# Kernel optimization log

Hardware: AMD Instinct MI355X
Metric: run time of the kernel (lower is better)

Reference implementation:

```python
import jax, jax.numpy as jnp
import numpy as np

EPS = 1e-5


def setup_inputs() -> dict:
    key = jax.random.key(0)
    k1, k2, k3, k4 = jax.random.split(key, 4)
    B, C, H, W = 32, 256, 64, 64
    x_real = jax.random.normal(k1, (B, C, H, W), dtype=jnp.float32)
    x_imag = jax.random.normal(k2, (B, C, H, W), dtype=jnp.float32)
    # per-channel 2x2 affine weight and 2-vector bias (module init is
    # 0.7071*I and zeros; we perturb so gradients are non-trivial)
    weight = (0.70710678 * jnp.eye(2, dtype=jnp.float32)[:, :, None]
              + 0.05 * jax.random.normal(k3, (2, 2, C), dtype=jnp.float32))
    bias = 0.05 * jax.random.normal(k4, (2, C), dtype=jnp.float32)
    return {"x_real": x_real, "x_imag": x_imag, "weight": weight, "bias": bias}


def reference(x_real, x_imag, weight, bias):
    # Complex BatchNorm (training-mode batch statistics).
    # x_*: [B, C, H, W]; stats reduced over (B, H, W) per channel C.
    axes = (0, 2, 3)
    mu_r = jnp.mean(x_real, axes)  # [C]
    mu_i = jnp.mean(x_imag, axes)  # [C]
    xr = x_real - mu_r[None, :, None, None]
    xi = x_imag - mu_i[None, :, None, None]

    # 2x2 covariance per channel, eps on the diagonal
    Vrr = jnp.mean(xr * xr, axes) + EPS  # [C]
    Vii = jnp.mean(xi * xi, axes) + EPS  # [C]
    Vri = jnp.mean(xr * xi, axes)        # [C]

    # Analytic inverse square root of the 2x2 SPD matrix [[Vrr,Vri],[Vri,Vii]]
    s = jnp.sqrt(Vrr * Vii - Vri * Vri)       # sqrt(det)
    t = jnp.sqrt(Vrr + Vii + 2.0 * s)         # sqrt(trace + 2 sqrt(det))
    inv_st = 1.0 / (s * t)
    Rrr = (Vii + s) * inv_st
    Rii = (Vrr + s) * inv_st
    Rri = -Vri * inv_st

    # Whitening (per-channel 2x2 matmul on (real, imag))
    cb = lambda v: v[None, :, None, None]
    xhat_r = cb(Rrr) * xr + cb(Rri) * xi
    xhat_i = cb(Rri) * xr + cb(Rii) * xi

    # Affine: out = W @ xhat + b, W: [2,2,C], b: [2,C]
    out_r = cb(weight[0, 0]) * xhat_r + cb(weight[0, 1]) * xhat_i + cb(bias[0])
    out_i = cb(weight[1, 0]) * xhat_r + cb(weight[1, 1]) * xhat_i + cb(bias[1])
    return jnp.stack([out_r, out_i], axis=0)  # [2, B, C, H, W]
```

## Files before the change

kernel.cpp:

```cpp
#include <hip/hip_runtime.h>
#include <math.h>

#define C_CH   256
#define HW     4096
#define B_N    32
#define N_PER_CH (B_N * HW)
#define N_TOT  ((size_t)B_N * C_CH * HW)
#define EPS_BN 1e-5f

typedef float f32x4 __attribute__((ext_vector_type(4)));

__global__ __launch_bounds__(1024) void cbn_fused(
    const float* __restrict__ xr, const float* __restrict__ xi,
    const float* __restrict__ weight,
    const float* __restrict__ bias,
    float* __restrict__ out)
{
    const int c = blockIdx.x;
    const int t = threadIdx.x;
    const f32x4* r4 = reinterpret_cast<const f32x4*>(xr);
    const f32x4* i4 = reinterpret_cast<const f32x4*>(xi);

    float sr = 0.f, si = 0.f, srr = 0.f, sii = 0.f, sri = 0.f;
#pragma unroll 4
    for (int j = 0; j < B_N; ++j) {
        const size_t idx = ((size_t)(j * C_CH + c) << 10) + t;
        const f32x4 a = r4[idx];
        const f32x4 b = i4[idx];
        sr  += a.x + a.y + a.z + a.w;
        si  += b.x + b.y + b.z + b.w;
        srr += a.x * a.x + a.y * a.y + a.z * a.z + a.w * a.w;
        sii += b.x * b.x + b.y * b.y + b.z * b.z + b.w * b.w;
        sri += a.x * b.x + a.y * b.y + a.z * b.z + a.w * b.w;
    }

#pragma unroll
    for (int off = 32; off > 0; off >>= 1) {
        sr  += __shfl_down(sr,  off);
        si  += __shfl_down(si,  off);
        srr += __shfl_down(srr, off);
        sii += __shfl_down(sii, off);
        sri += __shfl_down(sri, off);
    }

    __shared__ float red[5][16];
    __shared__ float scoef[6];
    const int wave = t >> 6;
    if ((t & 63) == 0) {
        red[0][wave] = sr;  red[1][wave] = si;
        red[2][wave] = srr; red[3][wave] = sii; red[4][wave] = sri;
    }
    __syncthreads();

    if (t < 64) {
        float v0 = 0.f, v1 = 0.f, v2 = 0.f, v3 = 0.f, v4 = 0.f;
        if (t < 16) {
            v0 = red[0][t]; v1 = red[1][t]; v2 = red[2][t];
            v3 = red[3][t]; v4 = red[4][t];
        }
#pragma unroll
        for (int off = 8; off > 0; off >>= 1) {
            v0 += __shfl_down(v0, off);
            v1 += __shfl_down(v1, off);
            v2 += __shfl_down(v2, off);
            v3 += __shfl_down(v3, off);
            v4 += __shfl_down(v4, off);
        }
        if (t == 0) {
            const float invN = 1.0f / (float)N_PER_CH;
            const float mur = v0 * invN;
            const float mui = v1 * invN;
            const float Vrr = v2 * invN - mur * mur + EPS_BN;
            const float Vii = v3 * invN - mui * mui + EPS_BN;
            const float Vri = v4 * invN - mur * mui;

            const float s      = sqrtf(Vrr * Vii - Vri * Vri);
            const float tt     = sqrtf(Vrr + Vii + 2.0f * s);
            const float inv_st = 1.0f / (s * tt);
            const float Rrr = (Vii + s) * inv_st;
            const float Rii = (Vrr + s) * inv_st;
            const float Rri = -Vri * inv_st;

            const float w00 = weight[0 * C_CH + c];
            const float w01 = weight[1 * C_CH + c];
            const float w10 = weight[2 * C_CH + c];
            const float w11 = weight[3 * C_CH + c];
            const float b0  = bias[c];
            const float b1  = bias[C_CH + c];

            const float Ar = w00 * Rrr + w01 * Rri;
            const float Br = w00 * Rri + w01 * Rii;
            const float Ai = w10 * Rrr + w11 * Rri;
            const float Bi = w10 * Rri + w11 * Rii;

            scoef[0] = Ar;
            scoef[1] = Br;
            scoef[2] = b0 - Ar * mur - Br * mui;
            scoef[3] = Ai;
            scoef[4] = Bi;
            scoef[5] = b1 - Ai * mur - Bi * mui;
        }
    }
    __syncthreads();

    const float Ar = scoef[0], Br = scoef[1], Cr = scoef[2];
    const float Ai = scoef[3], Bi = scoef[4], Ci = scoef[5];

    f32x4* o4 = reinterpret_cast<f32x4*>(out);
    const size_t n4 = N_TOT / 4;

#pragma unroll 4
    for (int j = 0; j < B_N; ++j) {
        const size_t idx = ((size_t)(j * C_CH + c) << 10) + t;
        const f32x4 a = __builtin_nontemporal_load(&r4[idx]);
        const f32x4 b = __builtin_nontemporal_load(&i4[idx]);
        f32x4 u, v;
        u.x = Ar * a.x + Br * b.x + Cr;
        u.y = Ar * a.y + Br * b.y + Cr;
        u.z = Ar * a.z + Br * b.z + Cr;
        u.w = Ar * a.w + Br * b.w + Cr;
        v.x = Ai * a.x + Bi * b.x + Ci;
        v.y = Ai * a.y + Bi * b.y + Ci;
        v.z = Ai * a.z + Bi * b.z + Ci;
        v.w = Ai * a.w + Bi * b.w + Ci;
        __builtin_nontemporal_store(u, &o4[idx]);
        __builtin_nontemporal_store(v, &o4[n4 + idx]);
    }
}

extern "C" void kernel_launch(void* const* d_in, const int* in_sizes, int n_in,
                              void* d_out, int out_size, void* d_ws, size_t ws_size,
                              hipStream_t stream) {
    const float* xr     = (const float*)d_in[0];
    const float* xi     = (const float*)d_in[1];
    const float* weight = (const float*)d_in[2];
    const float* bias   = (const float*)d_in[3];
    float* out = (float*)d_out;

    cbn_fused<<<C_CH, 1024, 0, stream>>>(xr, xi, weight, bias, out);
}
```

Measured before the change: 121.1 us.

## Keep part of each channel's input in registers and LDS between stats and apply passes

The first 10 batch slices per thread are held in registers and the next 4 in shared memory across the statistics pass, so the apply pass re-reads only the remaining 18 slices from global memory. This cuts second-pass HBM/L2 reads by roughly 14/32. In exchange it uses about 80 VGPRs of f32x4 for the cached slices and 128KB of LDS per block. With only 256 blocks of 1024 threads, occupancy is likely limited already, but the register pressure could force spills.

```diff
diff --git a/kernel.cpp b/kernel.cpp
--- a/kernel.cpp
+++ b/kernel.cpp
@@ -8,9 +8,12 @@
 #define N_TOT  ((size_t)B_N * C_CH * HW)
 #define EPS_BN 1e-5f
 
+#define JR 10
+#define JL 4
+
 typedef float f32x4 __attribute__((ext_vector_type(4)));
 
-__global__ __launch_bounds__(1024) void cbn_fused(
+__global__ __launch_bounds__(1024, 4) void cbn_fused(
     const float* __restrict__ xr, const float* __restrict__ xi,
     const float* __restrict__ weight,
     const float* __restrict__ bias,
@@ -21,9 +24,40 @@
     const f32x4* r4 = reinterpret_cast<const f32x4*>(xr);
     const f32x4* i4 = reinterpret_cast<const f32x4*>(xi);
 
+    __shared__ f32x4 lr[JL][1024];
+    __shared__ f32x4 li[JL][1024];
+    __shared__ float red[5][16];
+    __shared__ float scoef[6];
+
     float sr = 0.f, si = 0.f, srr = 0.f, sii = 0.f, sri = 0.f;
-#pragma unroll 4
-    for (int j = 0; j < B_N; ++j) {
+    f32x4 ra[JR], ia[JR];
+
+#pragma unroll
+    for (int j = 0; j < JR; ++j) {
+        const size_t idx = ((size_t)(j * C_CH + c) << 10) + t;
+        const f32x4 a = __builtin_nontemporal_load(&r4[idx]);
+        const f32x4 b = __builtin_nontemporal_load(&i4[idx]);
+        ra[j] = a; ia[j] = b;
+        sr  += a.x + a.y + a.z + a.w;
+        si  += b.x + b.y + b.z + b.w;
+        srr += a.x * a.x + a.y * a.y + a.z * a.z + a.w * a.w;
+        sii += b.x * b.x + b.y * b.y + b.z * b.z + b.w * b.w;
+        sri += a.x * b.x + a.y * b.y + a.z * b.z + a.w * b.w;
+    }
+#pragma unroll
+    for (int j = 0; j < JL; ++j) {
+        const size_t idx = ((size_t)((JR + j) * C_CH + c) << 10) + t;
+        const f32x4 a = __builtin_nontemporal_load(&r4[idx]);
+        const f32x4 b = __builtin_nontemporal_load(&i4[idx]);
+        lr[j][t] = a; li[j][t] = b;
+        sr  += a.x + a.y + a.z + a.w;
+        si  += b.x + b.y + b.z + b.w;
+        srr += a.x * a.x + a.y * a.y + a.z * a.z + a.w * a.w;
+        sii += b.x * b.x + b.y * b.y + b.z * b.z + b.w * b.w;
+        sri += a.x * b.x + a.y * b.y + a.z * b.z + a.w * b.w;
+    }
+#pragma unroll 2
+    for (int j = JR + JL; j < B_N; ++j) {
         const size_t idx = ((size_t)(j * C_CH + c) << 10) + t;
         const f32x4 a = r4[idx];
         const f32x4 b = i4[idx];
@@ -42,9 +76,6 @@
         sii += __shfl_down(sii, off);
         sri += __shfl_down(sri, off);
     }
-
-    __shared__ float red[5][16];
-    __shared__ float scoef[6];
     const int wave = t >> 6;
     if ((t & 63) == 0) {
         red[0][wave] = sr;  red[1][wave] = si;
@@ -109,8 +140,42 @@
     f32x4* o4 = reinterpret_cast<f32x4*>(out);
     const size_t n4 = N_TOT / 4;
 
-#pragma unroll 4
-    for (int j = 0; j < B_N; ++j) {
+#pragma unroll
+    for (int j = 0; j < JR; ++j) {
+        const size_t idx = ((size_t)(j * C_CH + c) << 10) + t;
+        const f32x4 a = ra[j];
+        const f32x4 b = ia[j];
+        f32x4 u, v;
+        u.x = Ar * a.x + Br * b.x + Cr;
+        u.y = Ar * a.y + Br * b.y + Cr;
+        u.z = Ar * a.z + Br * b.z + Cr;
+        u.w = Ar * a.w + Br * b.w + Cr;
+        v.x = Ai * a.x + Bi * b.x + Ci;
+        v.y = Ai * a.y + Bi * b.y + Ci;
+        v.z = Ai * a.z + Bi * b.z + Ci;
+        v.w = Ai * a.w + Bi * b.w + Ci;
+        __builtin_nontemporal_store(u, &o4[idx]);
+        __builtin_nontemporal_store(v, &o4[n4 + idx]);
+    }
+#pragma unroll
+    for (int j = 0; j < JL; ++j) {
+        const size_t idx = ((size_t)((JR + j) * C_CH + c) << 10) + t;
+        const f32x4 a = lr[j][t];
+        const f32x4 b = li[j][t];
+        f32x4 u, v;
+        u.x = Ar * a.x + Br * b.x + Cr;
+        u.y = Ar * a.y + Br * b.y + Cr;
+        u.z = Ar * a.z + Br * b.z + Cr;
+        u.w = Ar * a.w + Br * b.w + Cr;
+        v.x = Ai * a.x + Bi * b.x + Ci;
+        v.y = Ai * a.y + Bi * b.y + Ci;
+        v.z = Ai * a.z + Bi * b.z + Ci;
+        v.w = Ai * a.w + Bi * b.w + Ci;
+        __builtin_nontemporal_store(u, &o4[idx]);
+        __builtin_nontemporal_store(v, &o4[n4 + idx]);
+    }
+#pragma unroll 2
+    for (int j = JR + JL; j < B_N; ++j) {
         const size_t idx = ((size_t)(j * C_CH + c) << 10) + t;
         const f32x4 a = __builtin_nontemporal_load(&r4[idx]);
         const f32x4 b = __builtin_nontemporal_load(&i4[idx]);
```

After: 132.1 us. +9.0%, slower.

## Split channels into groups and pipeline stats and apply across five launches

Applied to the files above, without the earlier changes.

Replaces the single fused kernel (one 1024-thread block per channel) with five launches of 256 blocks of 512 threads. Each launch applies the normalization to one group of 64 channels while computing statistics for the next group. Each channel's statistics are split across 4 blocks and combined through a workspace buffer. The aim is to use more blocks and to reuse data while it is still in L2/MALL: the stats pass touches a group, and the apply pass reads that same group one launch later. In exchange it adds four extra kernel launch boundaries and depends on the workspace.

```diff
diff --git a/kernel.cpp b/kernel.cpp
--- a/kernel.cpp
+++ b/kernel.cpp
@@ -8,65 +8,42 @@
 #define N_TOT  ((size_t)B_N * C_CH * HW)
 #define EPS_BN 1e-5f
 
+#define GCH    64
+#define QS     8
+#define NT     512
+
 typedef float f32x4 __attribute__((ext_vector_type(4)));
 
-__global__ __launch_bounds__(1024) void cbn_fused(
+__global__ __launch_bounds__(NT) void cbn_epoch(
     const float* __restrict__ xr, const float* __restrict__ xi,
     const float* __restrict__ weight,
     const float* __restrict__ bias,
-    float* __restrict__ out)
+    float* __restrict__ out,
+    float* __restrict__ part,
+    const int apply_g, const int stats_g)
 {
-    const int c = blockIdx.x;
-    const int t = threadIdx.x;
+    const int blk = blockIdx.x;
+    const int t   = threadIdx.x;
     const f32x4* r4 = reinterpret_cast<const f32x4*>(xr);
     const f32x4* i4 = reinterpret_cast<const f32x4*>(xi);
 
-    float sr = 0.f, si = 0.f, srr = 0.f, sii = 0.f, sri = 0.f;
-#pragma unroll 4
-    for (int j = 0; j < B_N; ++j) {
-        const size_t idx = ((size_t)(j * C_CH + c) << 10) + t;
-        const f32x4 a = r4[idx];
-        const f32x4 b = i4[idx];
-        sr  += a.x + a.y + a.z + a.w;
-        si  += b.x + b.y + b.z + b.w;
-        srr += a.x * a.x + a.y * a.y + a.z * a.z + a.w * a.w;
-        sii += b.x * b.x + b.y * b.y + b.z * b.z + b.w * b.w;
-        sri += a.x * b.x + a.y * b.y + a.z * b.z + a.w * b.w;
-    }
+    __shared__ float sp[20];
+    __shared__ float scoef[6];
+    __shared__ float red[5][8];
 
-#pragma unroll
-    for (int off = 32; off > 0; off >>= 1) {
-        sr  += __shfl_down(sr,  off);
-        si  += __shfl_down(si,  off);
-        srr += __shfl_down(srr, off);
-        sii += __shfl_down(sii, off);
-        sri += __shfl_down(sri, off);
-    }
+    if (apply_g >= 0) {
+        const int ch = apply_g * GCH + (blk >> 2);
+        const int q  = blk & 3;
 
-    __shared__ float red[5][16];
-    __shared__ float scoef[6];
-    const int wave = t >> 6;
-    if ((t & 63) == 0) {
-        red[0][wave] = sr;  red[1][wave] = si;
-        red[2][wave] = srr; red[3][wave] = sii; red[4][wave] = sri;
-    }
-    __syncthreads();
+        if (t < 20) sp[t] = part[ch * 20 + t];
+        __syncthreads();
+        if (t == 0) {
+            const float v0 = sp[0] + sp[5]  + sp[10] + sp[15];
+            const float v1 = sp[1] + sp[6]  + sp[11] + sp[16];
+            const float v2 = sp[2] + sp[7]  + sp[12] + sp[17];
+            const float v3 = sp[3] + sp[8]  + sp[13] + sp[18];
+            const float v4 = sp[4] + sp[9]  + sp[14] + sp[19];
 
-    if (t < 64) {
-        float v0 = 0.f, v1 = 0.f, v2 = 0.f, v3 = 0.f, v4 = 0.f;
-        if (t < 16) {
-            v0 = red[0][t]; v1 = red[1][t]; v2 = red[2][t];
-            v3 = red[3][t]; v4 = red[4][t];
-        }
-#pragma unroll
-        for (int off = 8; off > 0; off >>= 1) {
-            v0 += __shfl_down(v0, off);
-            v1 += __shfl_down(v1, off);
-            v2 += __shfl_down(v2, off);
-            v3 += __shfl_down(v3, off);
-            v4 += __shfl_down(v4, off);
-        }
-        if (t == 0) {
             const float invN = 1.0f / (float)N_PER_CH;
             const float mur = v0 * invN;
             const float mui = v1 * invN;
@@ -81,12 +58,12 @@
             const float Rii = (Vrr + s) * inv_st;
             const float Rri = -Vri * inv_st;
 
-            const float w00 = weight[0 * C_CH + c];
-            const float w01 = weight[1 * C_CH + c];
-            const float w10 = weight[2 * C_CH + c];
-            const float w11 = weight[3 * C_CH + c];
-            const float b0  = bias[c];
-            const float b1  = bias[C_CH + c];
+            const float w00 = weight[0 * C_CH + ch];
+            const float w01 = weight[1 * C_CH + ch];
+            const float w10 = weight[2 * C_CH + ch];
+            const float w11 = weight[3 * C_CH + ch];
+            const float b0  = bias[ch];
+            const float b1  = bias[C_CH + ch];
 
             const float Ar = w00 * Rrr + w01 * Rri;
             const float Br = w00 * Rri + w01 * Rii;
@@ -100,31 +77,81 @@
             scoef[4] = Bi;
             scoef[5] = b1 - Ai * mur - Bi * mui;
         }
+        __syncthreads();
+
+        const float Ar = scoef[0], Br = scoef[1], Cr = scoef[2];
+        const float Ai = scoef[3], Bi = scoef[4], Ci = scoef[5];
+
+        f32x4* o4 = reinterpret_cast<f32x4*>(out);
+        const size_t n4 = N_TOT / 4;
+
+#pragma unroll 2
+        for (int j = q * QS; j < q * QS + QS; ++j) {
+            const size_t base = ((size_t)(j * C_CH + ch) << 10);
+#pragma unroll
+            for (int k = 0; k < 2; ++k) {
+                const size_t idx = base + (size_t)k * NT + t;
+                const f32x4 a = __builtin_nontemporal_load(&r4[idx]);
+                const f32x4 b = __builtin_nontemporal_load(&i4[idx]);
+                f32x4 u, v;
+                u.x = Ar * a.x + Br * b.x + Cr;
+                u.y = Ar * a.y + Br * b.y + Cr;
+                u.z = Ar * a.z + Br * b.z + Cr;
+                u.w = Ar * a.w + Br * b.w + Cr;
+                v.x = Ai * a.x + Bi * b.x + Ci;
+                v.y = Ai * a.y + Bi * b.y + Ci;
+                v.z = Ai * a.z + Bi * b.z + Ci;
+                v.w = Ai * a.w + Bi * b.w + Ci;
+                __builtin_nontemporal_store(u, &o4[idx]);
+                __builtin_nontemporal_store(v, &o4[n4 + idx]);
+            }
+        }
     }
-    __syncthreads();
 
-    const float Ar = scoef[0], Br = scoef[1], Cr = scoef[2];
-    const float Ai = scoef[3], Bi = scoef[4], Ci = scoef[5];
+    if (stats_g >= 0) {
+        const int ch = stats_g * GCH + (blk >> 2);
+        const int q  = blk & 3;
 
-    f32x4* o4 = reinterpret_cast<f32x4*>(out);
-    const size_t n4 = N_TOT / 4;
+        float sr = 0.f, si = 0.f, srr = 0.f, sii = 0.f, sri = 0.f;
+#pragma unroll 2
+        for (int j = q * QS; j < q * QS + QS; ++j) {
+            const size_t base = ((size_t)(j * C_CH + ch) << 10);
+#pragma unroll
+            for (int k = 0; k < 2; ++k) {
+                const size_t idx = base + (size_t)k * NT + t;
+                const f32x4 a = r4[idx];
+                const f32x4 b = i4[idx];
+                sr  += a.x + a.y + a.z + a.w;
+                si  += b.x + b.y + b.z + b.w;
+                srr += a.x * a.x + a.y * a.y + a.z * a.z + a.w * a.w;
+                sii += b.x * b.x + b.y * b.y + b.z * b.z + b.w * b.w;
+                sri += a.x * b.x + a.y * b.y + a.z * b.z + a.w * b.w;
+            }
+        }
 
-#pragma unroll 4
-    for (int j = 0; j < B_N; ++j) {
-        const size_t idx = ((size_t)(j * C_CH + c) << 10) + t;
-        const f32x4 a = __builtin_nontemporal_load(&r4[idx]);
-        const f32x4 b = __builtin_nontemporal_load(&i4[idx]);
-        f32x4 u, v;
-        u.x = Ar * a.x + Br * b.x + Cr;
-        u.y = Ar * a.y + Br * b.y + Cr;
-        u.z = Ar * a.z + Br * b.z + Cr;
-        u.w = Ar * a.w + Br * b.w + Cr;
-        v.x = Ai * a.x + Bi * b.x + Ci;
-        v.y = Ai * a.y + Bi * b.y + Ci;
-        v.z = Ai * a.z + Bi * b.z + Ci;
-        v.w = Ai * a.w + Bi * b.w + Ci;
-        __builtin_nontemporal_store(u, &o4[idx]);
-        __builtin_nontemporal_store(v, &o4[n4 + idx]);
+#pragma unroll
+        for (int off = 32; off > 0; off >>= 1) {
+            sr  += __shfl_down(sr,  off);
+            si  += __shfl_down(si,  off);
+            srr += __shfl_down(srr, off);
+            sii += __shfl_down(sii, off);
+            sri += __shfl_down(sri, off);
+        }
+        const int wave = t >> 6;
+        if ((t & 63) == 0) {
+            red[0][wave] = sr;  red[1][wave] = si;
+            red[2][wave] = srr; red[3][wave] = sii; red[4][wave] = sri;
+        }
+        __syncthreads();
+        if (t == 0) {
+#pragma unroll
+            for (int k = 0; k < 5; ++k) {
+                float acc = red[k][0];
+#pragma unroll
+                for (int w = 1; w < NT / 64; ++w) acc += red[k][w];
+                part[ch * 20 + q * 5 + k] = acc;
+            }
+        }
     }
 }
 
@@ -135,7 +162,12 @@
     const float* xi     = (const float*)d_in[1];
     const float* weight = (const float*)d_in[2];
     const float* bias   = (const float*)d_in[3];
-    float* out = (float*)d_out;
+    float* out  = (float*)d_out;
+    float* part = (float*)d_ws;
 
-    cbn_fused<<<C_CH, 1024, 0, stream>>>(xr, xi, weight, bias, out);
+    cbn_epoch<<<256, NT, 0, stream>>>(xr, xi, weight, bias, out, part, -1, 0);
+    cbn_epoch<<<256, NT, 0, stream>>>(xr, xi, weight, bias, out, part,  0, 1);
+    cbn_epoch<<<256, NT, 0, stream>>>(xr, xi, weight, bias, out, part,  1, 2);
+    cbn_epoch<<<256, NT, 0, stream>>>(xr, xi, weight, bias, out, part,  2, 3);
+    cbn_epoch<<<256, NT, 0, stream>>>(xr, xi, weight, bias, out, part,  3, -1);
 }
```

Measured after the change: 130.2 us. +7.5%, slower.

## Split channel across block pair and retain inputs in registers and LDS

Applied to the files above, without the earlier changes.

Each channel is now handled by two 256-thread blocks, each covering half the batch. The pair exchanges partial statistics through a workspace flag handshake with release/acquire atomics. Each block keeps 6 of its 16 batch slices in registers and 2 in LDS, so the second pass rereads only the remaining 8 slices from global memory. This cuts HBM reads in the apply pass and doubles the block count. In exchange it relies on both blocks of a pair being co-resident to avoid deadlock, and it adds a memset launch.

```diff
diff --git a/kernel.cpp b/kernel.cpp
--- a/kernel.cpp
+++ b/kernel.cpp
@@ -8,31 +8,77 @@
 #define N_TOT  ((size_t)B_N * C_CH * HW)
 #define EPS_BN 1e-5f
 
+#define HALF   16
+#define RS     6
+#define LS     2
+
 typedef float f32x4 __attribute__((ext_vector_type(4)));
 
-__global__ __launch_bounds__(1024) void cbn_fused(
+__global__ __launch_bounds__(256) void cbn_ret(
     const float* __restrict__ xr, const float* __restrict__ xi,
     const float* __restrict__ weight,
     const float* __restrict__ bias,
-    float* __restrict__ out)
+    float* __restrict__ out,
+    float* __restrict__ part,
+    int*   __restrict__ flag)
 {
-    const int c = blockIdx.x;
-    const int t = threadIdx.x;
+    const int b  = blockIdx.x;
+    const int c  = b >> 1;
+    const int h  = b & 1;
+    const int t  = threadIdx.x;
+    const int j0 = h * HALF;
+
     const f32x4* r4 = reinterpret_cast<const f32x4*>(xr);
     const f32x4* i4 = reinterpret_cast<const f32x4*>(xi);
 
+    __shared__ f32x4 lsr[LS][1024];
+    __shared__ f32x4 lsi[LS][1024];
+    __shared__ float red[5][4];
+    __shared__ float scoef[6];
+
     float sr = 0.f, si = 0.f, srr = 0.f, sii = 0.f, sri = 0.f;
-#pragma unroll 4
-    for (int j = 0; j < B_N; ++j) {
-        const size_t idx = ((size_t)(j * C_CH + c) << 10) + t;
-        const f32x4 a = r4[idx];
-        const f32x4 b = i4[idx];
-        sr  += a.x + a.y + a.z + a.w;
-        si  += b.x + b.y + b.z + b.w;
-        srr += a.x * a.x + a.y * a.y + a.z * a.z + a.w * a.w;
-        sii += b.x * b.x + b.y * b.y + b.z * b.z + b.w * b.w;
-        sri += a.x * b.x + a.y * b.y + a.z * b.z + a.w * b.w;
-    }
+    f32x4 ra[RS][4], ia[RS][4];
+
+#define ACC(a, bb)                                              \
+    sr  += a.x + a.y + a.z + a.w;                               \
+    si  += bb.x + bb.y + bb.z + bb.w;                           \
+    srr += a.x*a.x + a.y*a.y + a.z*a.z + a.w*a.w;               \
+    sii += bb.x*bb.x + bb.y*bb.y + bb.z*bb.z + bb.w*bb.w;       \
+    sri += a.x*bb.x + a.y*bb.y + a.z*bb.z + a.w*bb.w;
+
+#pragma unroll
+    for (int j = 0; j < RS; ++j) {
+        const size_t base = ((size_t)((j0 + j) * C_CH + c) << 10);
+#pragma unroll
+        for (int k = 0; k < 4; ++k) {
+            const f32x4 a  = __builtin_nontemporal_load(&r4[base + k * 256 + t]);
+            const f32x4 bb = __builtin_nontemporal_load(&i4[base + k * 256 + t]);
+            ra[j][k] = a; ia[j][k] = bb;
+            ACC(a, bb)
+        }
+    }
+#pragma unroll
+    for (int j = 0; j < LS; ++j) {
+        const size_t base = ((size_t)((j0 + RS + j) * C_CH + c) << 10);
+#pragma unroll
+        for (int k = 0; k < 4; ++k) {
+            const f32x4 a  = __builtin_nontemporal_load(&r4[base + k * 256 + t]);
+            const f32x4 bb = __builtin_nontemporal_load(&i4[base + k * 256 + t]);
+            lsr[j][k * 256 + t] = a; lsi[j][k * 256 + t] = bb;
+            ACC(a, bb)
+        }
+    }
+#pragma unroll 2
+    for (int j = RS + LS; j < HALF; ++j) {
+        const size_t base = ((size_t)((j0 + j) * C_CH + c) << 10);
+#pragma unroll
+        for (int k = 0; k < 4; ++k) {
+            const f32x4 a  = r4[base + k * 256 + t];
+            const f32x4 bb = i4[base + k * 256 + t];
+            ACC(a, bb)
+        }
+    }
+#undef ACC
 
 #pragma unroll
     for (int off = 32; off > 0; off >>= 1) {
@@ -42,9 +88,6 @@
         sii += __shfl_down(sii, off);
         sri += __shfl_down(sri, off);
     }
-
-    __shared__ float red[5][16];
-    __shared__ float scoef[6];
     const int wave = t >> 6;
     if ((t & 63) == 0) {
         red[0][wave] = sr;  red[1][wave] = si;
@@ -52,54 +95,64 @@
     }
     __syncthreads();
 
-    if (t < 64) {
-        float v0 = 0.f, v1 = 0.f, v2 = 0.f, v3 = 0.f, v4 = 0.f;
-        if (t < 16) {
-            v0 = red[0][t]; v1 = red[1][t]; v2 = red[2][t];
-            v3 = red[3][t]; v4 = red[4][t];
-        }
-#pragma unroll
-        for (int off = 8; off > 0; off >>= 1) {
-            v0 += __shfl_down(v0, off);
-            v1 += __shfl_down(v1, off);
-            v2 += __shfl_down(v2, off);
-            v3 += __shfl_down(v3, off);
-            v4 += __shfl_down(v4, off);
-        }
-        if (t == 0) {
-            const float invN = 1.0f / (float)N_PER_CH;
-            const float mur = v0 * invN;
-            const float mui = v1 * invN;
-            const float Vrr = v2 * invN - mur * mur + EPS_BN;
-            const float Vii = v3 * invN - mui * mui + EPS_BN;
-            const float Vri = v4 * invN - mur * mui;
-
-            const float s      = sqrtf(Vrr * Vii - Vri * Vri);
-            const float tt     = sqrtf(Vrr + Vii + 2.0f * s);
-            const float inv_st = 1.0f / (s * tt);
-            const float Rrr = (Vii + s) * inv_st;
-            const float Rii = (Vrr + s) * inv_st;
-            const float Rri = -Vri * inv_st;
-
-            const float w00 = weight[0 * C_CH + c];
-            const float w01 = weight[1 * C_CH + c];
-            const float w10 = weight[2 * C_CH + c];
-            const float w11 = weight[3 * C_CH + c];
-            const float b0  = bias[c];
-            const float b1  = bias[C_CH + c];
-
-            const float Ar = w00 * Rrr + w01 * Rri;
-            const float Br = w00 * Rri + w01 * Rii;
-            const float Ai = w10 * Rrr + w11 * Rri;
-            const float Bi = w10 * Rri + w11 * Rii;
-
-            scoef[0] = Ar;
-            scoef[1] = Br;
-            scoef[2] = b0 - Ar * mur - Br * mui;
-            scoef[3] = Ai;
-            scoef[4] = Bi;
-            scoef[5] = b1 - Ai * mur - Bi * mui;
-        }
+    if (t == 0) {
+        float own[5];
+#pragma unroll
+        for (int k = 0; k < 5; ++k)
+            own[k] = red[k][0] + red[k][1] + red[k][2] + red[k][3];
+
+#pragma unroll
+        for (int k = 0; k < 5; ++k)
+            __hip_atomic_store(&part[b * 5 + k], own[k],
+                               __ATOMIC_RELAXED, __HIP_MEMORY_SCOPE_AGENT);
+        __hip_atomic_store(&flag[b], 1,
+                           __ATOMIC_RELEASE, __HIP_MEMORY_SCOPE_AGENT);
+
+        const int ob = (c << 1) | (h ^ 1);
+        while (__hip_atomic_load(&flag[ob],
+                                 __ATOMIC_ACQUIRE, __HIP_MEMORY_SCOPE_AGENT) == 0) {
+            __builtin_amdgcn_s_sleep(8);
+        }
+        float v[5];
+#pragma unroll
+        for (int k = 0; k < 5; ++k) {
+            const float oth = __hip_atomic_load(&part[ob * 5 + k],
+                                                __ATOMIC_RELAXED, __HIP_MEMORY_SCOPE_AGENT);
+            v[k] = own[k] + oth;
+        }
+
+        const float invN = 1.0f / (float)N_PER_CH;
+        const float mur = v[0] * invN;
+        const float mui = v[1] * invN;
+        const float Vrr = v[2] * invN - mur * mur + EPS_BN;
+        const float Vii = v[3] * invN - mui * mui + EPS_BN;
+        const float Vri = v[4] * invN - mur * mui;
+
+        const float s      = sqrtf(Vrr * Vii - Vri * Vri);
+        const float tt     = sqrtf(Vrr + Vii + 2.0f * s);
+        const float inv_st = 1.0f / (s * tt);
+        const float Rrr = (Vii + s) * inv_st;
+        const float Rii = (Vrr + s) * inv_st;
+        const float Rri = -Vri * inv_st;
+
+        const float w00 = weight[0 * C_CH + c];
+        const float w01 = weight[1 * C_CH + c];
+        const float w10 = weight[2 * C_CH + c];
+        const float w11 = weight[3 * C_CH + c];
+        const float b0  = bias[c];
+        const float b1  = bias[C_CH + c];
+
+        const float Ar = w00 * Rrr + w01 * Rri;
+        const float Br = w00 * Rri + w01 * Rii;
+        const float Ai = w10 * Rrr + w11 * Rri;
+        const float Bi = w10 * Rri + w11 * Rii;
+
+        scoef[0] = Ar;
+        scoef[1] = Br;
+        scoef[2] = b0 - Ar * mur - Br * mui;
+        scoef[3] = Ai;
+        scoef[4] = Bi;
+        scoef[5] = b1 - Ai * mur - Bi * mui;
     }
     __syncthreads();
 
@@ -109,23 +162,46 @@
     f32x4* o4 = reinterpret_cast<f32x4*>(out);
     const size_t n4 = N_TOT / 4;
 
-#pragma unroll 4
-    for (int j = 0; j < B_N; ++j) {
-        const size_t idx = ((size_t)(j * C_CH + c) << 10) + t;
-        const f32x4 a = __builtin_nontemporal_load(&r4[idx]);
-        const f32x4 b = __builtin_nontemporal_load(&i4[idx]);
-        f32x4 u, v;
-        u.x = Ar * a.x + Br * b.x + Cr;
-        u.y = Ar * a.y + Br * b.y + Cr;
-        u.z = Ar * a.z + Br * b.z + Cr;
-        u.w = Ar * a.w + Br * b.w + Cr;
-        v.x = Ai * a.x + Bi * b.x + Ci;
-        v.y = Ai * a.y + Bi * b.y + Ci;
-        v.z = Ai * a.z + Bi * b.z + Ci;
-        v.w = Ai * a.w + Bi * b.w + Ci;
-        __builtin_nontemporal_store(u, &o4[idx]);
-        __builtin_nontemporal_store(v, &o4[n4 + idx]);
-    }
+#define APPLY_STORE(a, bb, idx)                                 \
+    {   f32x4 u, w_;                                            \
+        u.x = Ar*a.x + Br*bb.x + Cr;  u.y = Ar*a.y + Br*bb.y + Cr; \
+        u.z = Ar*a.z + Br*bb.z + Cr;  u.w = Ar*a.w + Br*bb.w + Cr; \
+        w_.x = Ai*a.x + Bi*bb.x + Ci; w_.y = Ai*a.y + Bi*bb.y + Ci;\
+        w_.z = Ai*a.z + Bi*bb.z + Ci; w_.w = Ai*a.w + Bi*bb.w + Ci;\
+        __builtin_nontemporal_store(u,  &o4[idx]);              \
+        __builtin_nontemporal_store(w_, &o4[n4 + idx]); }
+
+#pragma unroll
+    for (int j = 0; j < RS; ++j) {
+        const size_t base = ((size_t)((j0 + j) * C_CH + c) << 10);
+#pragma unroll
+        for (int k = 0; k < 4; ++k) {
+            const f32x4 a  = ra[j][k];
+            const f32x4 bb = ia[j][k];
+            APPLY_STORE(a, bb, base + k * 256 + t)
+        }
+    }
+#pragma unroll
+    for (int j = 0; j < LS; ++j) {
+        const size_t base = ((size_t)((j0 + RS + j) * C_CH + c) << 10);
+#pragma unroll
+        for (int k = 0; k < 4; ++k) {
+            const f32x4 a  = lsr[j][k * 256 + t];
+            const f32x4 bb = lsi[j][k * 256 + t];
+            APPLY_STORE(a, bb, base + k * 256 + t)
+        }
+    }
+#pragma unroll 2
+    for (int j = RS + LS; j < HALF; ++j) {
+        const size_t base = ((size_t)((j0 + j) * C_CH + c) << 10);
+#pragma unroll
+        for (int k = 0; k < 4; ++k) {
+            const f32x4 a  = __builtin_nontemporal_load(&r4[base + k * 256 + t]);
+            const f32x4 bb = __builtin_nontemporal_load(&i4[base + k * 256 + t]);
+            APPLY_STORE(a, bb, base + k * 256 + t)
+        }
+    }
+#undef APPLY_STORE
 }
 
 extern "C" void kernel_launch(void* const* d_in, const int* in_sizes, int n_in,
@@ -137,5 +213,10 @@
     const float* bias   = (const float*)d_in[3];
     float* out = (float*)d_out;
 
-    cbn_fused<<<C_CH, 1024, 0, stream>>>(xr, xi, weight, bias, out);
+    int*   flag = (int*)d_ws;
+    float* part = (float*)((char*)d_ws + 2048);
+
+    hipMemsetAsync(d_ws, 0, 2048, stream);
+
+    cbn_ret<<<512, 256, 0, stream>>>(xr, xi, weight, bias, out, part, flag);
 }
```

New measurement: 125.5 us. 3.6% more time.
